# Performance work log

Measured on AMD Instinct MI355X. Metric: run time of the kernel, lower is better.

The kernel has to match this reference:

```python
import jax, jax.numpy as jnp
import numpy as np

P = 8  # patch_size
MD = 32  # metric_dim


def setup_inputs() -> dict:
    key = jax.random.key(0)
    ks = jax.random.split(key, 7)
    b, c, H, W = 4, 3, 512, 512
    s = 1.0 / np.sqrt(MD)
    return {
        "x": jax.random.normal(ks[0], (b, c, H, W), dtype=jnp.float32),
        "conv_w": jax.random.normal(ks[1], (MD, c, P, P), dtype=jnp.float32) * (1.0 / np.sqrt(c * P * P)),
        "conv_b": jax.random.normal(ks[2], (MD,), dtype=jnp.float32) * 0.02,
        "proj_w": jax.random.normal(ks[3], (3 * MD, MD), dtype=jnp.float32) * s,
        "proj_b": jax.random.normal(ks[4], (3 * MD,), dtype=jnp.float32) * 0.02,
        "deconv_w": jax.random.normal(ks[5], (MD, 3, P, P), dtype=jnp.float32) * s,
        "deconv_b": jax.random.normal(ks[6], (3,), dtype=jnp.float32) * 0.02,
    }


def reference(x, conv_w, conv_b, proj_w, proj_b, deconv_w, deconv_b):
    b, c, H, W = x.shape
    hh, ww = H // P, W // P
    # patch embed: Conv2d(kernel=stride=P) == block-reshape + einsum
    xp = x.reshape(b, c, hh, P, ww, P)
    tok = jnp.einsum('bchpwq,ocpq->bohw', xp, conv_w) + conv_b[None, :, None, None]
    # 'b c h w -> b (h w) c'
    tok = tok.reshape(b, MD, hh * ww).transpose(0, 2, 1)  # [b, N, MD]
    xs = tok @ proj_w.T + proj_b
    q, k, v = jnp.split(xs, 3, axis=-1)
    # full NxN QK^T with zeroed diagonal
    lp = jnp.einsum('bnd,bmd->bnm', q, k)
    n = lp.shape[-1]
    i = jnp.arange(n)
    lp = lp.at[:, i, i].set(0.0)
    # cos-phase interference, then matmul with V
    inter = jnp.cos((2.0 * jnp.pi) * lp) @ v  # [b, N, MD]
    # 'b (h w) c -> b c h w'
    inter = inter.transpose(0, 2, 1).reshape(b, MD, hh, ww)
    # ConvTranspose2d(kernel=stride=P) == einsum + block-unreshape
    out = jnp.einsum('bihw,iopq->bohpwq', inter, deconv_w).reshape(b, deconv_w.shape[1], H, W)
    out = out + deconv_b[None, :, None, None]
    return out
```

## Files before the change

### kernel.cpp

```cpp
#include <hip/hip_runtime.h>
#include <hip/hip_bf16.h>

#define NTOK   4096
#define NBATCH 4
#define SPLIT  8

typedef short bf16x8 __attribute__((ext_vector_type(8)));
typedef float f32x4  __attribute__((ext_vector_type(4)));

static __device__ inline short f2bf(float x) {
    __hip_bfloat16 h = __float2bfloat16(x);
    return __builtin_bit_cast(short, h);
}
static __device__ inline float bf2f(short s) {
    return __bfloat162float(__builtin_bit_cast(__hip_bfloat16, s));
}
static __device__ inline f32x4 mfma16(bf16x8 a, bf16x8 b, f32x4 c) {
    return __builtin_amdgcn_mfma_f32_16x16x32_bf16(a, b, c, 0, 0, 0);
}

__global__ __launch_bounds__(256) void k_embed(
    const float* __restrict__ x,  const float* __restrict__ cw,
    const float* __restrict__ cb, const float* __restrict__ pw,
    const float* __restrict__ pb,
    short* __restrict__ qh, short* __restrict__ ql,
    short* __restrict__ kh, short* __restrict__ kl,
    float* __restrict__ vv)
{
    __shared__ float tok_lds[64][33];
    const int tid  = threadIdx.x;
    const int og   = tid >> 6;
    const int tl   = tid & 63;
    const int bx   = blockIdx.x;
    const int b    = bx >> 6;
    const int hrow = bx & 63;
    const int n    = hrow * 64 + tl;

    float acc[8];
#pragma unroll
    for (int i = 0; i < 8; ++i) acc[i] = cb[og * 8 + i];

    const float* xb = x + (size_t)b * 3 * 512 * 512;
#pragma unroll
    for (int c = 0; c < 3; ++c) {
        float4 xr[16];
#pragma unroll
        for (int p = 0; p < 8; ++p) {
            const float* row = xb + ((size_t)c * 512 + hrow * 8 + p) * 512 + tl * 8;
            xr[p * 2]     = *(const float4*)row;
            xr[p * 2 + 1] = *(const float4*)(row + 4);
        }
#pragma unroll
        for (int oo = 0; oo < 8; ++oo) {
            const float* wrow = cw + ((size_t)(og * 8 + oo) * 3 + c) * 64;
            float s = 0.f;
#pragma unroll
            for (int j = 0; j < 16; ++j) {
                float4 wv = *(const float4*)(wrow + j * 4);
                s += xr[j].x * wv.x + xr[j].y * wv.y + xr[j].z * wv.z + xr[j].w * wv.w;
            }
            acc[oo] += s;
        }
    }
#pragma unroll
    for (int oo = 0; oo < 8; ++oo) tok_lds[tl][og * 8 + oo] = acc[oo];
    __syncthreads();
    float tok[32];
#pragma unroll
    for (int d = 0; d < 32; ++d) tok[d] = tok_lds[tl][d];

    const int toff = (b * NTOK + n) * 32;
#pragma unroll
    for (int g2 = 0; g2 < 6; ++g2) {
        int jb = og * 24 + g2 * 4;
        float r[4];
#pragma unroll
        for (int l2 = 0; l2 < 4; ++l2) {
            int j = jb + l2;
            float s = pb[j];
            const float* prow = pw + j * 32;
#pragma unroll
            for (int d4 = 0; d4 < 8; ++d4) {
                float4 wv = *(const float4*)(prow + d4 * 4);
                s += tok[d4 * 4 + 0] * wv.x + tok[d4 * 4 + 1] * wv.y
                   + tok[d4 * 4 + 2] * wv.z + tok[d4 * 4 + 3] * wv.w;
            }
            r[l2] = s;
        }
        if (jb < 64) {
            short hs[4], ls2[4];
#pragma unroll
            for (int l2 = 0; l2 < 4; ++l2) {
                hs[l2]  = f2bf(r[l2]);
                ls2[l2] = f2bf(r[l2] - bf2f(hs[l2]));
            }
            int off = (jb < 32) ? jb : (jb - 32);
            short* dh = (jb < 32) ? qh : kh;
            short* dl = (jb < 32) ? ql : kl;
            *(short4*)(dh + toff + off) = make_short4(hs[0], hs[1], hs[2], hs[3]);
            *(short4*)(dl + toff + off) = make_short4(ls2[0], ls2[1], ls2[2], ls2[3]);
        } else {
            *(float4*)(vv + toff + (jb - 64)) = make_float4(r[0], r[1], r[2], r[3]);
        }
    }
}

__global__ __launch_bounds__(256) void k_varr(
    const float* __restrict__ vv, short* __restrict__ varr)
{
    const int t = threadIdx.x, l = t & 63, w = t >> 6;
    const int g = l >> 4, r16 = l & 15;
    const int bx = blockIdx.x;
    const int b = bx >> 5, cg = bx & 31;
    const int c = cg * 4 + w;
    const float* vb = vv + ((size_t)b * NTOK + c * 32) * 32;
#pragma unroll
    for (int dt = 0; dt < 2; ++dt) {
        bf16x8 hv, lv;
#pragma unroll
        for (int j = 0; j < 8; ++j) {
            int m = (j < 4) ? (4 * g + j) : (16 + 4 * g + (j - 4));
            float xv = vb[m * 32 + dt * 16 + r16];
            short hsj = f2bf(xv);
            hv[j] = hsj;
            lv[j] = f2bf(xv - bf2f(hsj));
        }
        size_t base = ((size_t)b * 128 + c) * 2048 + (size_t)dt * 1024 + (size_t)l * 8;
        *(bf16x8*)(varr + base)       = hv;
        *(bf16x8*)(varr + base + 512) = lv;
    }
}

__global__ __launch_bounds__(256, 3) void k_attn(
    const short* __restrict__ qh, const short* __restrict__ ql,
    const short* __restrict__ kh, const short* __restrict__ kl,
    const short* __restrict__ varr, float* __restrict__ part)
{
    const int t = threadIdx.x, l = t & 63, w = t >> 6;
    const int g = l >> 4, r16 = l & 15;
    const int bx = blockIdx.x;
    const int s = bx & 7, b = (bx >> 3) & 3, nb = bx >> 5;
    const int n0 = nb * 128 + w * 32;
    const int qkbase = b * NTOK * 32;

    bf16x8 qfh[2], qfl[2];
#pragma unroll
    for (int nt = 0; nt < 2; ++nt) {
        int ro = qkbase + (n0 + nt * 16 + r16) * 32 + g * 8;
        qfh[nt] = *(const bf16x8*)(qh + ro);
        qfl[nt] = *(const bf16x8*)(ql + ro);
    }
    f32x4 acc[2][2];
#pragma unroll
    for (int nt = 0; nt < 2; ++nt)
#pragma unroll
        for (int dt = 0; dt < 2; ++dt)
            acc[nt][dt] = (f32x4){0.f, 0.f, 0.f, 0.f};

    for (int ch = 0; ch < 16; ++ch) {
        const int mc = s * 512 + ch * 32;
        bf16x8 kfh[2], kfl[2];
#pragma unroll
        for (int mh = 0; mh < 2; ++mh) {
            int ro = qkbase + (mc + mh * 16 + r16) * 32 + g * 8;
            kfh[mh] = *(const bf16x8*)(kh + ro);
            kfl[mh] = *(const bf16x8*)(kl + ro);
        }
        const short* vbase = varr + ((size_t)(b * 128 + (mc >> 5))) * 2048;
        bf16x8 vf00 = *(const bf16x8*)(vbase + l * 8);
        bf16x8 vf01 = *(const bf16x8*)(vbase + 512 + l * 8);
        bf16x8 vf10 = *(const bf16x8*)(vbase + 1024 + l * 8);
        bf16x8 vf11 = *(const bf16x8*)(vbase + 1536 + l * 8);

        bf16x8 pah[2], pal[2];
#pragma unroll
        for (int nt = 0; nt < 2; ++nt) {
            f32x4 sa = (f32x4){0.f, 0.f, 0.f, 0.f};
            f32x4 sb = (f32x4){0.f, 0.f, 0.f, 0.f};
            sa = mfma16(kfh[0], qfh[nt], sa);
            sa = mfma16(kfh[0], qfl[nt], sa);
            sa = mfma16(kfl[0], qfh[nt], sa);
            sb = mfma16(kfh[1], qfh[nt], sb);
            sb = mfma16(kfh[1], qfl[nt], sb);
            sb = mfma16(kfl[1], qfh[nt], sb);
#pragma unroll
            for (int r = 0; r < 4; ++r) {
                float xa = sa[r];
                float ca = __builtin_amdgcn_cosf(xa - floorf(xa));
                short ha = f2bf(ca);
                pah[nt][r] = ha;
                pal[nt][r] = f2bf(ca - bf2f(ha));
                float xb = sb[r];
                float cb2 = __builtin_amdgcn_cosf(xb - floorf(xb));
                short hb = f2bf(cb2);
                pah[nt][r + 4] = hb;
                pal[nt][r + 4] = f2bf(cb2 - bf2f(hb));
            }
        }
#pragma unroll
        for (int nt = 0; nt < 2; ++nt) {
            acc[nt][0] = mfma16(pah[nt], vf00, acc[nt][0]);
            acc[nt][0] = mfma16(pah[nt], vf01, acc[nt][0]);
            acc[nt][0] = mfma16(pal[nt], vf00, acc[nt][0]);
            acc[nt][1] = mfma16(pah[nt], vf10, acc[nt][1]);
            acc[nt][1] = mfma16(pah[nt], vf11, acc[nt][1]);
            acc[nt][1] = mfma16(pal[nt], vf10, acc[nt][1]);
        }
    }
    float* pbp = part + ((size_t)(s * NBATCH + b) * NTOK) * 32;
#pragma unroll
    for (int nt = 0; nt < 2; ++nt)
#pragma unroll
        for (int dt = 0; dt < 2; ++dt)
#pragma unroll
            for (int r = 0; r < 4; ++r)
                pbp[(n0 + nt * 16 + 4 * g + r) * 32 + dt * 16 + r16] = acc[nt][dt][r];
}

__global__ __launch_bounds__(256) void k_deconv(
    const float* __restrict__ part,
    const short* __restrict__ qh, const short* __restrict__ ql,
    const short* __restrict__ kh, const short* __restrict__ kl,
    const float* __restrict__ vv,
    const float* __restrict__ dw, const float* __restrict__ db,
    float* __restrict__ out)
{
    __shared__ float vt2[32][64];
    __shared__ float dots[64][4];
    __shared__ float coef[64];
    const int tid  = threadIdx.x;
    const int og   = tid >> 6;
    const int tl   = tid & 63;
    const int bx   = blockIdx.x;
    const int b    = bx >> 6;
    const int hrow = bx & 63;
    const int n    = hrow * 64 + tl;
    const int toff = (b * NTOK + n) * 32;

    {
        const float* vrow = vv + toff + og * 8;
#pragma unroll
        for (int i = 0; i < 8; ++i) vt2[og * 8 + i][tl] = vrow[i];
        float dp = 0.f;
        const short* qhp = qh + toff + og * 8;
        const short* qlp = ql + toff + og * 8;
        const short* khp = kh + toff + og * 8;
        const short* klp = kl + toff + og * 8;
#pragma unroll
        for (int i = 0; i < 8; ++i) {
            float qv = bf2f(qhp[i]) + bf2f(qlp[i]);
            float kv = bf2f(khp[i]) + bf2f(klp[i]);
            dp += qv * kv;
        }
        dots[tl][og] = dp;
    }
    __syncthreads();
    if (og == 0) {
        float sd = (dots[tl][0] + dots[tl][1]) + (dots[tl][2] + dots[tl][3]);
        coef[tl] = 1.f - __builtin_amdgcn_cosf(sd - floorf(sd));
    }
    __syncthreads();

    float ir[32];
#pragma unroll
    for (int d = 0; d < 32; ++d) ir[d] = 0.f;
#pragma unroll
    for (int s = 0; s < SPLIT; ++s) {
        const float* ip = part + ((size_t)(s * NBATCH + b) * NTOK + n) * 32;
#pragma unroll
        for (int d4 = 0; d4 < 8; ++d4) {
            float4 t4 = *(const float4*)(ip + d4 * 4);
            ir[d4 * 4 + 0] += t4.x; ir[d4 * 4 + 1] += t4.y;
            ir[d4 * 4 + 2] += t4.z; ir[d4 * 4 + 3] += t4.w;
        }
    }
    const float cf = coef[tl];
#pragma unroll
    for (int d = 0; d < 32; ++d) ir[d] += cf * vt2[d][tl];

    float oa[48];
#pragma unroll
    for (int g2 = 0; g2 < 12; ++g2) {
        int jj = og * 48 + g2 * 4;
        float bv = db[jj >> 6];
        oa[g2 * 4 + 0] = bv; oa[g2 * 4 + 1] = bv;
        oa[g2 * 4 + 2] = bv; oa[g2 * 4 + 3] = bv;
    }
#pragma unroll
    for (int i = 0; i < 32; ++i) {
        float iv = ir[i];
#pragma unroll
        for (int g2 = 0; g2 < 12; ++g2) {
            int jj = og * 48 + g2 * 4;
            float4 wv = *(const float4*)(dw + ((size_t)i * 3 + (jj >> 6)) * 64 + (jj & 63));
            oa[g2 * 4 + 0] += iv * wv.x; oa[g2 * 4 + 1] += iv * wv.y;
            oa[g2 * 4 + 2] += iv * wv.z; oa[g2 * 4 + 3] += iv * wv.w;
        }
    }
#pragma unroll
    for (int g2 = 0; g2 < 12; ++g2) {
        int jj = og * 48 + g2 * 4;
        int o = jj >> 6, pq = jj & 63, p = pq >> 3, qq = pq & 7;
        *(float4*)(out + (((size_t)b * 3 + o) * 512 + hrow * 8 + p) * 512 + tl * 8 + qq)
            = make_float4(oa[g2 * 4 + 0], oa[g2 * 4 + 1], oa[g2 * 4 + 2], oa[g2 * 4 + 3]);
    }
}

extern "C" void kernel_launch(void* const* d_in, const int* in_sizes, int n_in,
                              void* d_out, int out_size, void* d_ws, size_t ws_size,
                              hipStream_t stream)
{
    const float* x  = (const float*)d_in[0];
    const float* cw = (const float*)d_in[1];
    const float* cb = (const float*)d_in[2];
    const float* pw = (const float*)d_in[3];
    const float* pb = (const float*)d_in[4];
    const float* dw = (const float*)d_in[5];
    const float* db = (const float*)d_in[6];
    float* out = (float*)d_out;

    char* wsb = (char*)d_ws;
    const size_t MB = 1u << 20;
    short* qh   = (short*)(wsb + 0 * MB);
    short* ql   = (short*)(wsb + 1 * MB);
    short* kh   = (short*)(wsb + 2 * MB);
    short* kl   = (short*)(wsb + 3 * MB);
    float* vv   = (float*)(wsb + 4 * MB);
    short* varr = (short*)(wsb + 6 * MB);
    float* part = (float*)(wsb + 8 * MB);

    hipLaunchKernelGGL(k_embed, dim3(256), dim3(256), 0, stream,
                       x, cw, cb, pw, pb, qh, ql, kh, kl, vv);
    hipLaunchKernelGGL(k_varr, dim3(128), dim3(256), 0, stream, vv, varr);
    hipLaunchKernelGGL(k_attn, dim3(1024), dim3(256), 0, stream,
                       qh, ql, kh, kl, varr, part);
    hipLaunchKernelGGL(k_deconv, dim3(256), dim3(256), 0, stream,
                       part, qh, ql, kh, kl, vv, dw, db, out);
}
```

Before: 170.7 us.

## Split deconv into reduce and deconv kernels, move diagonal coef into embed

The diagonal correction coefficient is now computed in the embed kernel from fp32 q/k held in shared memory, rather than being rebuilt from hi/lo bf16 pairs in the deconv kernel. The split-K partial reduction moves into a separate fully parallel kernel that writes an intermediate buffer. The deconv kernel is restructured so each wave produces whole 8-wide output rows, with 512 threads per block. k_varr now stages through shared memory so its global stores are coalesced, and it uses more blocks. This adds a kernel launch and an extra round-trip through the intermediate buffer in exchange for better parallelism and memory access patterns.

```diff
diff --git a/kernel.cpp b/kernel.cpp
--- a/kernel.cpp
+++ b/kernel.cpp
@@ -25,9 +25,10 @@
     const float* __restrict__ pb,
     short* __restrict__ qh, short* __restrict__ ql,
     short* __restrict__ kh, short* __restrict__ kl,
-    float* __restrict__ vv)
+    float* __restrict__ vv, float* __restrict__ coef)
 {
     __shared__ float tok_lds[64][33];
+    __shared__ float qk_lds[64][65];
     const int tid  = threadIdx.x;
     const int og   = tid >> 6;
     const int tl   = tid & 63;
@@ -88,6 +89,8 @@
             r[l2] = s;
         }
         if (jb < 64) {
+#pragma unroll
+            for (int l2 = 0; l2 < 4; ++l2) qk_lds[tl][jb + l2] = r[l2];
             short hs[4], ls2[4];
 #pragma unroll
             for (int l2 = 0; l2 < 4; ++l2) {
@@ -103,32 +106,44 @@
             *(float4*)(vv + toff + (jb - 64)) = make_float4(r[0], r[1], r[2], r[3]);
         }
     }
+    __syncthreads();
+    if (og == 0) {
+        float dp = 0.f;
+#pragma unroll
+        for (int d = 0; d < 32; ++d) dp += qk_lds[tl][d] * qk_lds[tl][32 + d];
+        coef[b * NTOK + n] = 1.f - __builtin_amdgcn_cosf(dp - floorf(dp));
+    }
 }
 
 __global__ __launch_bounds__(256) void k_varr(
     const float* __restrict__ vv, short* __restrict__ varr)
 {
-    const int t = threadIdx.x, l = t & 63, w = t >> 6;
-    const int g = l >> 4, r16 = l & 15;
-    const int bx = blockIdx.x;
-    const int b = bx >> 5, cg = bx & 31;
-    const int c = cg * 4 + w;
+    __shared__ short lds[2048];
+    const int tid = threadIdx.x;
+    const int bx  = blockIdx.x;
+    const int b   = bx >> 7, c = bx & 127;
     const float* vb = vv + ((size_t)b * NTOK + c * 32) * 32;
-#pragma unroll
-    for (int dt = 0; dt < 2; ++dt) {
-        bf16x8 hv, lv;
-#pragma unroll
-        for (int j = 0; j < 8; ++j) {
-            int m = (j < 4) ? (4 * g + j) : (16 + 4 * g + (j - 4));
-            float xv = vb[m * 32 + dt * 16 + r16];
-            short hsj = f2bf(xv);
-            hv[j] = hsj;
-            lv[j] = f2bf(xv - bf2f(hsj));
-        }
-        size_t base = ((size_t)b * 128 + c) * 2048 + (size_t)dt * 1024 + (size_t)l * 8;
-        *(bf16x8*)(varr + base)       = hv;
-        *(bf16x8*)(varr + base + 512) = lv;
-    }
+
+    const int m  = tid >> 3;
+    const int d0 = (tid & 7) * 4;
+    float4 v4 = *(const float4*)(vb + tid * 4);
+    float vd[4] = {v4.x, v4.y, v4.z, v4.w};
+#pragma unroll
+    for (int l2 = 0; l2 < 4; ++l2) {
+        int d = d0 + l2;
+        int dt = d >> 4, r16 = d & 15;
+        int g, j;
+        if (m < 16) { g = m >> 2; j = m & 3; }
+        else        { g = (m - 16) >> 2; j = 4 + ((m - 16) & 3); }
+        int lane = g * 16 + r16;
+        short hv = f2bf(vd[l2]);
+        short lv = f2bf(vd[l2] - bf2f(hv));
+        lds[dt * 1024 + 0 * 512 + lane * 8 + j] = hv;
+        lds[dt * 1024 + 1 * 512 + lane * 8 + j] = lv;
+    }
+    __syncthreads();
+    *(bf16x8*)(varr + ((size_t)b * 128 + c) * 2048 + tid * 8)
+        = *(const bf16x8*)(lds + tid * 8);
 }
 
 __global__ __launch_bounds__(256, 3) void k_attn(
@@ -217,92 +232,67 @@
                 pbp[(n0 + nt * 16 + 4 * g + r) * 32 + dt * 16 + r16] = acc[nt][dt][r];
 }
 
-__global__ __launch_bounds__(256) void k_deconv(
-    const float* __restrict__ part,
-    const short* __restrict__ qh, const short* __restrict__ ql,
-    const short* __restrict__ kh, const short* __restrict__ kl,
-    const float* __restrict__ vv,
-    const float* __restrict__ dw, const float* __restrict__ db,
-    float* __restrict__ out)
-{
-    __shared__ float vt2[32][64];
-    __shared__ float dots[64][4];
-    __shared__ float coef[64];
+__global__ __launch_bounds__(256) void k_reduce(
+    const float* __restrict__ part, const float* __restrict__ vv,
+    const float* __restrict__ coef, float* __restrict__ inter)
+{
+    const int idx = blockIdx.x * 256 + threadIdx.x;
+    const int g = idx >> 3, d4 = idx & 7;
+    const float* p0 = part + (size_t)g * 32 + d4 * 4;
+    float4 s = make_float4(0.f, 0.f, 0.f, 0.f);
+#pragma unroll
+    for (int sp = 0; sp < SPLIT; ++sp) {
+        float4 t = *(const float4*)(p0 + (size_t)sp * (NBATCH * NTOK * 32));
+        s.x += t.x; s.y += t.y; s.z += t.z; s.w += t.w;
+    }
+    const float cf = coef[g];
+    float4 v4 = *(const float4*)(vv + (size_t)g * 32 + d4 * 4);
+    s.x += cf * v4.x; s.y += cf * v4.y; s.z += cf * v4.z; s.w += cf * v4.w;
+    *(float4*)(inter + (size_t)g * 32 + d4 * 4) = s;
+}
+
+__global__ __launch_bounds__(512) void k_deconv(
+    const float* __restrict__ inter, const float* __restrict__ dw,
+    const float* __restrict__ db, float* __restrict__ out)
+{
     const int tid  = threadIdx.x;
-    const int og   = tid >> 6;
-    const int tl   = tid & 63;
+    const int wv   = tid >> 6;
+    const int lane = tid & 63;
     const int bx   = blockIdx.x;
     const int b    = bx >> 6;
     const int hrow = bx & 63;
-    const int n    = hrow * 64 + tl;
-    const int toff = (b * NTOK + n) * 32;
-
-    {
-        const float* vrow = vv + toff + og * 8;
-#pragma unroll
-        for (int i = 0; i < 8; ++i) vt2[og * 8 + i][tl] = vrow[i];
-        float dp = 0.f;
-        const short* qhp = qh + toff + og * 8;
-        const short* qlp = ql + toff + og * 8;
-        const short* khp = kh + toff + og * 8;
-        const short* klp = kl + toff + og * 8;
-#pragma unroll
-        for (int i = 0; i < 8; ++i) {
-            float qv = bf2f(qhp[i]) + bf2f(qlp[i]);
-            float kv = bf2f(khp[i]) + bf2f(klp[i]);
-            dp += qv * kv;
-        }
-        dots[tl][og] = dp;
-    }
-    __syncthreads();
-    if (og == 0) {
-        float sd = (dots[tl][0] + dots[tl][1]) + (dots[tl][2] + dots[tl][3]);
-        coef[tl] = 1.f - __builtin_amdgcn_cosf(sd - floorf(sd));
-    }
-    __syncthreads();
+    const int n    = hrow * 64 + lane;
 
     float ir[32];
-#pragma unroll
-    for (int d = 0; d < 32; ++d) ir[d] = 0.f;
-#pragma unroll
-    for (int s = 0; s < SPLIT; ++s) {
-        const float* ip = part + ((size_t)(s * NBATCH + b) * NTOK + n) * 32;
-#pragma unroll
-        for (int d4 = 0; d4 < 8; ++d4) {
-            float4 t4 = *(const float4*)(ip + d4 * 4);
-            ir[d4 * 4 + 0] += t4.x; ir[d4 * 4 + 1] += t4.y;
-            ir[d4 * 4 + 2] += t4.z; ir[d4 * 4 + 3] += t4.w;
-        }
-    }
-    const float cf = coef[tl];
-#pragma unroll
-    for (int d = 0; d < 32; ++d) ir[d] += cf * vt2[d][tl];
-
-    float oa[48];
-#pragma unroll
-    for (int g2 = 0; g2 < 12; ++g2) {
-        int jj = og * 48 + g2 * 4;
-        float bv = db[jj >> 6];
-        oa[g2 * 4 + 0] = bv; oa[g2 * 4 + 1] = bv;
-        oa[g2 * 4 + 2] = bv; oa[g2 * 4 + 3] = bv;
-    }
-#pragma unroll
-    for (int i = 0; i < 32; ++i) {
-        float iv = ir[i];
-#pragma unroll
-        for (int g2 = 0; g2 < 12; ++g2) {
-            int jj = og * 48 + g2 * 4;
-            float4 wv = *(const float4*)(dw + ((size_t)i * 3 + (jj >> 6)) * 64 + (jj & 63));
-            oa[g2 * 4 + 0] += iv * wv.x; oa[g2 * 4 + 1] += iv * wv.y;
-            oa[g2 * 4 + 2] += iv * wv.z; oa[g2 * 4 + 3] += iv * wv.w;
-        }
-    }
-#pragma unroll
-    for (int g2 = 0; g2 < 12; ++g2) {
-        int jj = og * 48 + g2 * 4;
-        int o = jj >> 6, pq = jj & 63, p = pq >> 3, qq = pq & 7;
-        *(float4*)(out + (((size_t)b * 3 + o) * 512 + hrow * 8 + p) * 512 + tl * 8 + qq)
-            = make_float4(oa[g2 * 4 + 0], oa[g2 * 4 + 1], oa[g2 * 4 + 2], oa[g2 * 4 + 3]);
+    const float* ip = inter + ((size_t)(b * NTOK + n)) * 32;
+#pragma unroll
+    for (int d4 = 0; d4 < 8; ++d4) {
+        float4 t4 = *(const float4*)(ip + d4 * 4);
+        ir[d4 * 4 + 0] = t4.x; ir[d4 * 4 + 1] = t4.y;
+        ir[d4 * 4 + 2] = t4.z; ir[d4 * 4 + 3] = t4.w;
+    }
+#pragma unroll
+    for (int rr = 0; rr < 3; ++rr) {
+        const int rho = wv * 3 + rr;
+        const int o = rho >> 3, p = rho & 7;
+        const float bv = db[o];
+        float a8[8];
+#pragma unroll
+        for (int q = 0; q < 8; ++q) a8[q] = bv;
+        const float* wbase = dw + o * 64 + p * 8;
+#pragma unroll
+        for (int i = 0; i < 32; ++i) {
+            float4 w0 = *(const float4*)(wbase + (size_t)i * 192);
+            float4 w1 = *(const float4*)(wbase + (size_t)i * 192 + 4);
+            const float iv = ir[i];
+            a8[0] += iv * w0.x; a8[1] += iv * w0.y;
+            a8[2] += iv * w0.z; a8[3] += iv * w0.w;
+            a8[4] += iv * w1.x; a8[5] += iv * w1.y;
+            a8[6] += iv * w1.z; a8[7] += iv * w1.w;
+        }
+        float* op = out + (((size_t)(b * 3 + o) * 512) + hrow * 8 + p) * 512 + lane * 8;
+        *(float4*)op       = make_float4(a8[0], a8[1], a8[2], a8[3]);
+        *(float4*)(op + 4) = make_float4(a8[4], a8[5], a8[6], a8[7]);
     }
 }
 
@@ -321,19 +311,23 @@
 
     char* wsb = (char*)d_ws;
     const size_t MB = 1u << 20;
-    short* qh   = (short*)(wsb + 0 * MB);
-    short* ql   = (short*)(wsb + 1 * MB);
-    short* kh   = (short*)(wsb + 2 * MB);
-    short* kl   = (short*)(wsb + 3 * MB);
-    float* vv   = (float*)(wsb + 4 * MB);
-    short* varr = (short*)(wsb + 6 * MB);
-    float* part = (float*)(wsb + 8 * MB);
+    short* qh    = (short*)(wsb + 0 * MB);
+    short* ql    = (short*)(wsb + 1 * MB);
+    short* kh    = (short*)(wsb + 2 * MB);
+    short* kl    = (short*)(wsb + 3 * MB);
+    float* vv    = (float*)(wsb + 4 * MB);
+    short* varr  = (short*)(wsb + 6 * MB);
+    float* part  = (float*)(wsb + 8 * MB);
+    float* coef  = (float*)(wsb + 24 * MB);
+    float* inter = (float*)(wsb + 25 * MB);
 
     hipLaunchKernelGGL(k_embed, dim3(256), dim3(256), 0, stream,
-                       x, cw, cb, pw, pb, qh, ql, kh, kl, vv);
-    hipLaunchKernelGGL(k_varr, dim3(128), dim3(256), 0, stream, vv, varr);
+                       x, cw, cb, pw, pb, qh, ql, kh, kl, vv, coef);
+    hipLaunchKernelGGL(k_varr, dim3(512), dim3(256), 0, stream, vv, varr);
     hipLaunchKernelGGL(k_attn, dim3(1024), dim3(256), 0, stream,
                        qh, ql, kh, kl, varr, part);
-    hipLaunchKernelGGL(k_deconv, dim3(256), dim3(256), 0, stream,
-                       part, qh, ql, kh, kl, vv, dw, db, out);
-}
+    hipLaunchKernelGGL(k_reduce, dim3(512), dim3(256), 0, stream,
+                       part, vv, coef, inter);
+    hipLaunchKernelGGL(k_deconv, dim3(256), dim3(512), 0, stream,
+                       inter, dw, db, out);
+}
```

Measured after the change: 145.6 us. -14.7%, faster.
